# Optimization experiments

Measured on AMD Instinct MI355X. Metric: run time of the kernel, lower is better.

Reference implementation:

```python
import jax, jax.numpy as jnp
import numpy as np

NUM_SAMPLES = 10
MIN_DIST_PTS = 8
TOP_K = 10
GRID_SIZE = 4
GAP = 0.1


def sample_line_points(seg):
    # seg: [N,2,2] (endpoints, ij coords). Vectorized version of the per-group linspace loop.
    lengths = jnp.linalg.norm(seg[:, 0] - seg[:, 1], axis=1)
    n_samp = jnp.clip(jnp.floor(lengths / MIN_DIST_PTS), 2, NUM_SAMPLES)  # [N]
    t = jnp.arange(NUM_SAMPLES, dtype=seg.dtype)  # [S]
    interval = (seg[:, 1] - seg[:, 0]) / (n_samp[:, None] - 1)  # [N,2]
    pts = seg[:, None, 0, :] + t[None, :, None] * interval[:, None, :]  # [N,S,2]
    valid = t[None, :] < n_samp[:, None]  # [N,S]
    pts = jnp.where(valid[..., None], pts, 0.0)  # original zero-pads invalid samples
    return pts, valid


def grid_sample_norm(desc, pts, img_size):
    # desc: [D,Hc,Wc]; pts: [P,2] (i,j) pixel coords in image of size img_size=(H,W).
    # Replicates kornia normalize_pixel_coordinates + F.grid_sample(align_corners=False,
    # bilinear, zero padding), then L2-normalize along D.
    D, Hc, Wc = desc.shape
    H, W = img_size
    gx = 2.0 * pts[:, 1] / (W - 1) - 1.0
    gy = 2.0 * pts[:, 0] / (H - 1) - 1.0
    ix = ((gx + 1.0) * Wc - 1.0) / 2.0
    iy = ((gy + 1.0) * Hc - 1.0) / 2.0
    x0 = jnp.floor(ix)
    y0 = jnp.floor(iy)
    wx1 = ix - x0
    wy1 = iy - y0
    x0i = x0.astype(jnp.int32)
    y0i = y0.astype(jnp.int32)

    def gather(yi, xi):
        inb = (xi >= 0) & (xi < Wc) & (yi >= 0) & (yi < Hc)
        v = desc[:, jnp.clip(yi, 0, Hc - 1), jnp.clip(xi, 0, Wc - 1)]  # [D,P]
        return v * inb

    v = (gather(y0i, x0i) * (1 - wy1) * (1 - wx1)
         + gather(y0i, x0i + 1) * (1 - wy1) * wx1
         + gather(y0i + 1, x0i) * wy1 * (1 - wx1)
         + gather(y0i + 1, x0i + 1) * wy1 * wx1)
    nrm = jnp.linalg.norm(v, axis=0, keepdims=True)
    return v / jnp.maximum(nrm, 1e-12)


def needleman_wunsch(scores):
    # scores: [B,n,m]. Row-wise scan; the within-row dependency
    # v[j+1]=max(v[j], max(prev[j+1], prev[j]+s)) is a prefix-max (cummax).
    b, n, m = scores.shape
    s = scores - GAP
    init = jnp.zeros((b, m + 1), s.dtype)

    def step(prev, row):  # prev [B,m+1], row [B,m]
        a = jnp.maximum(prev[:, 1:], prev[:, :-1] + row)
        new = jnp.maximum(jax.lax.cummax(a, axis=1), 0.0)
        return jnp.concatenate([jnp.zeros((b, 1), s.dtype), new], axis=1), None

    final, _ = jax.lax.scan(step, init, jnp.swapaxes(s, 0, 1))
    return final[:, -1]


def nw_candidate_scores(scores):
    # scores: [N1,N2,S,S] -> (nw [N1,2k], topk [N1,k])
    ls1 = jnp.max(scores, axis=3)
    v1 = ls1 != -1
    ls1 = jnp.where(v1, ls1, 0.0).sum(2) / v1.sum(2)
    ls2 = jnp.max(scores, axis=2)
    v2 = ls2 != -1
    ls2 = jnp.where(v2, ls2, 0.0).sum(2) / v2.sum(2)
    line_scores = (ls1 + ls2) / 2
    topk = jnp.argsort(line_scores, axis=1)[:, -TOP_K:]  # [N1,k]
    top_scores = jnp.take_along_axis(scores, topk[:, :, None, None], axis=1)  # [N1,k,S,S]
    top_scores = jnp.concatenate([top_scores, jnp.flip(top_scores, axis=-1)], axis=1)  # [N1,2k,S,S]
    N1, t2k, n, m = top_scores.shape
    nw = needleman_wunsch(top_scores.reshape(N1 * t2k, n, m)).reshape(N1, t2k)
    return nw, topk


def filter_and_match(scores):
    nw, topk = nw_candidate_scores(scores)
    t2k = nw.shape[1]
    best = jnp.argmax(nw, axis=1) % (t2k // 2)
    return jnp.take_along_axis(topk, best[:, None], axis=1)[:, 0]


def compute_scores(line_seg1, line_seg2, desc1, desc2):
    S = NUM_SAMPLES
    img1 = (desc1.shape[2] * GRID_SIZE, desc1.shape[3] * GRID_SIZE)
    img2 = (desc2.shape[2] * GRID_SIZE, desc2.shape[3] * GRID_SIZE)
    pts1, val1 = sample_line_points(line_seg1)
    pts2, val2 = sample_line_points(line_seg2)
    d1 = grid_sample_norm(desc1[0], pts1.reshape(-1, 2), img1)  # [D, N1*S]
    d2 = grid_sample_norm(desc2[0], pts2.reshape(-1, 2), img2)  # [D, N2*S]
    sc = d1.T @ d2  # [N1*S, N2*S]
    sc = jnp.where(val1.reshape(-1)[:, None], sc, -1.0)
    sc = jnp.where(val2.reshape(-1)[None, :], sc, -1.0)
    N1, N2 = line_seg1.shape[0], line_seg2.shape[0]
    return sc.reshape(N1, S, N2, S).transpose(0, 2, 1, 3)  # [N1,N2,S,S]


def reference(line_seg1, line_seg2, desc1, desc2):
    scores = compute_scores(line_seg1, line_seg2, desc1, desc2)
    matches = filter_and_match(scores)
    # cross check
    matches2 = filter_and_match(scores.transpose(1, 0, 3, 2))
    mutual = matches2[matches] == jnp.arange(line_seg1.shape[0])
    return jnp.where(mutual, matches, -1).astype(jnp.int32)


def setup_inputs() -> dict:
    key = jax.random.key(0)
    k1, k2, k3, k4 = jax.random.split(key, 4)
    IMG = 512.0
    line_seg1 = jax.random.uniform(k1, (512, 2, 2), dtype=jnp.float32) * (IMG - 1.0)
    line_seg2 = jax.random.uniform(k2, (512, 2, 2), dtype=jnp.float32) * (IMG - 1.0)
    desc1 = jax.random.normal(k3, (1, 128, 128, 128), dtype=jnp.float32)
    desc2 = jax.random.normal(k4, (1, 128, 128, 128), dtype=jnp.float32)
    return {"line_seg1": line_seg1, "line_seg2": line_seg2, "desc1": desc1, "desc2": desc2}
```

## Files before the change

kernel.cpp:

```cpp
#include <hip/hip_runtime.h>
#include <cmath>

#define NL 512
#define SS 10
#define DD 128
#define HWC (128 * 128)

typedef _Float16 f16x8 __attribute__((ext_vector_type(8)));
typedef float f32x4 __attribute__((ext_vector_type(4)));

__device__ __forceinline__ void gload_lds16(const void* g, void* l)
{
    __builtin_amdgcn_global_load_lds(
        (__attribute__((address_space(1))) void*)const_cast<void*>(g),
        (__attribute__((address_space(3))) void*)l, 16, 0, 0);
}

__global__ __launch_bounds__(256) void transpose_kernel(
    const float* __restrict__ in1, const float* __restrict__ in2,
    float* __restrict__ out1, float* __restrict__ out2, int* __restrict__ cnt)
{
    if (blockIdx.x == 0 && blockIdx.y == 0 && blockIdx.z == 0 &&
        threadIdx.x == 0 && threadIdx.y == 0)
        atomicExch(cnt, 0);
    const float* in = blockIdx.z ? in2 : in1;
    float* out = blockIdx.z ? out2 : out1;
    __shared__ float tile[32][33];
    int hw0 = blockIdx.x * 32;
    int d0 = blockIdx.y * 32;
    int tx = threadIdx.x, ty = threadIdx.y;
#pragma unroll
    for (int j = 0; j < 32; j += 8)
        tile[ty + j][tx] = in[(size_t)(d0 + ty + j) * HWC + hw0 + tx];
    __syncthreads();
#pragma unroll
    for (int j = 0; j < 32; j += 8)
        out[(size_t)(hw0 + ty + j) * DD + d0 + tx] = tile[tx][ty + j];
}

__device__ __forceinline__ float fetchd(const float* __restrict__ dt, int y, int x, int d)
{
    bool inb = (x >= 0) && (x < 128) && (y >= 0) && (y < 128);
    int yc = y < 0 ? 0 : (y > 127 ? 127 : y);
    int xc = x < 0 ? 0 : (x > 127 ? 127 : x);
    float v = dt[((size_t)(yc * 128 + xc)) * DD + d];
    return inb ? v : 0.0f;
}

__global__ __launch_bounds__(640) void sample_kernel(
    const float* __restrict__ seg1, const float* __restrict__ seg2,
    const float* __restrict__ dt1, const float* __restrict__ dt2,
    float* __restrict__ dd1, float* __restrict__ dd2,
    _Float16* __restrict__ h1, _Float16* __restrict__ m1,
    _Float16* __restrict__ h2, _Float16* __restrict__ m2,
    int* __restrict__ v1, int* __restrict__ v2)
{
#pragma clang fp contract(off)
    int L = blockIdx.x;
    int img = blockIdx.y;
    const float* seg = img ? seg2 : seg1;
    const float* dt = img ? dt2 : dt1;
    float* dd = img ? dd2 : dd1;
    _Float16* ph = img ? h2 : h1;
    _Float16* pm = img ? m2 : m1;
    int* vv = img ? v2 : v1;

    float p0y = seg[L * 4 + 0], p0x = seg[L * 4 + 1];
    float p1y = seg[L * 4 + 2], p1x = seg[L * 4 + 3];
    float dy = p0y - p1y, dx = p0x - p1x;
    float len = sqrtf(dy * dy + dx * dx);
    float nf = floorf(len / 8.0f);
    nf = fminf(fmaxf(nf, 2.0f), 10.0f);
    int ni = (int)nf;
    float ivy = (p1y - p0y) / (nf - 1.0f);
    float ivx = (p1x - p0x) / (nf - 1.0f);

    int t = threadIdx.x >> 6;
    int lane = threadIdx.x & 63;
    int pt = L * SS + t;
    bool val = t < ni;
    int d0 = lane, d1 = lane + 64;
    float o0 = 0.0f, o1 = 0.0f;
    if (val) {
        float py = p0y + (float)t * ivy;
        float px = p0x + (float)t * ivx;
        float gx = 2.0f * px / 511.0f - 1.0f;
        float gy = 2.0f * py / 511.0f - 1.0f;
        float ix = ((gx + 1.0f) * 128.0f - 1.0f) / 2.0f;
        float iy = ((gy + 1.0f) * 128.0f - 1.0f) / 2.0f;
        float x0f = floorf(ix), y0f = floorf(iy);
        float wx = ix - x0f, wy = iy - y0f;
        int x0 = (int)x0f, y0 = (int)y0f;
        float a00 = fetchd(dt, y0, x0, d0),         b00 = fetchd(dt, y0, x0, d1);
        float a01 = fetchd(dt, y0, x0 + 1, d0),     b01 = fetchd(dt, y0, x0 + 1, d1);
        float a10 = fetchd(dt, y0 + 1, x0, d0),     b10 = fetchd(dt, y0 + 1, x0, d1);
        float a11 = fetchd(dt, y0 + 1, x0 + 1, d0), b11 = fetchd(dt, y0 + 1, x0 + 1, d1);
        float omwx = 1.0f - wx, omwy = 1.0f - wy;
        float va = a00 * omwy * omwx + a01 * omwy * wx + a10 * wy * omwx + a11 * wy * wx;
        float vb = b00 * omwy * omwx + b01 * omwy * wx + b10 * wy * omwx + b11 * wy * wx;
        float s = va * va + vb * vb;
#pragma unroll
        for (int m = 1; m < 64; m <<= 1) s += __shfl_xor(s, m);
        float nrm = sqrtf(s);
        o0 = va / fmaxf(nrm, 1e-12f);
        o1 = vb / fmaxf(nrm, 1e-12f);
    }
    dd[(size_t)pt * DD + d0] = o0;
    dd[(size_t)pt * DD + d1] = o1;
    float xs0 = o0 * 256.0f;
    _Float16 hh0 = (_Float16)xs0;
    _Float16 mm0 = (_Float16)(xs0 - (float)hh0);
    float xs1 = o1 * 256.0f;
    _Float16 hh1 = (_Float16)xs1;
    _Float16 mm1 = (_Float16)(xs1 - (float)hh1);
    int po0 = ((pt >> 4) << 11) + ((d0 >> 3) << 7) + ((pt & 15) << 3) + (d0 & 7);
    int po1 = ((pt >> 4) << 11) + ((d1 >> 3) << 7) + ((pt & 15) << 3) + (d1 & 7);
    ph[po0] = hh0; pm[po0] = mm0;
    ph[po1] = hh1; pm[po1] = mm1;
    if (lane == 0) vv[pt] = val ? 1 : 0;
}

__device__ __forceinline__ void stage_ks(
    const _Float16* __restrict__ ah, const _Float16* __restrict__ am,
    const _Float16* __restrict__ bh, const _Float16* __restrict__ bm,
    int bi, int bj, int ks, int wave, int lane, char* dst)
{
#pragma unroll
    for (int c = 0; c < 10; ++c) {
        int chunk = wave * 10 + c;
        int side = chunk >= 20;
        int rem = side ? chunk - 20 : chunk;
        int plane = rem >= 10;
        int pb = plane ? rem - 10 : rem;
        const _Float16* base = side ? (plane ? bm : bh) : (plane ? am : ah);
        size_t off = ((size_t)((side ? bj : bi) * 10 + pb) << 11) + (ks << 9) + (lane << 3);
        gload_lds16(base + off, dst + (chunk << 10));
    }
}

__global__ __launch_bounds__(256, 2) void gemm_ls_kernel(
    const _Float16* __restrict__ ah_, const _Float16* __restrict__ am_,
    const _Float16* __restrict__ bh_, const _Float16* __restrict__ bm_,
    const int* __restrict__ v1, const int* __restrict__ v2,
    float* __restrict__ ls, float* __restrict__ lsT)
{
    __shared__ __align__(16) char smem[122880];
    int tid = threadIdx.x;
    int wave = tid >> 6, lane = tid & 63;
    int wr = wave >> 1, wc = wave & 1;

    int flat = blockIdx.x;
    int xcd = flat & 7, n = flat >> 3;
    int bi = (xcd >> 1) * 8 + (n >> 4);
    int bj = (xcd & 1) * 16 + (n & 15);

    int fro = ((lane >> 4) << 8) + ((lane & 15) << 4);

    f32x4 zz = {0.0f, 0.0f, 0.0f, 0.0f};
    f32x4 acc[5][5];
#pragma unroll
    for (int i = 0; i < 5; ++i)
#pragma unroll
        for (int j = 0; j < 5; ++j) acc[i][j] = zz;

    stage_ks(ah_, am_, bh_, bm_, bi, bj, 0, wave, lane, smem);
    stage_ks(ah_, am_, bh_, bm_, bi, bj, 1, wave, lane, smem + 40960);

#pragma unroll 1
    for (int ks = 0; ks < 4; ++ks) {
        char* buf = smem + 40960 * (ks % 3);
        if (ks < 2) {
            stage_ks(ah_, am_, bh_, bm_, bi, bj, ks + 2, wave, lane,
                     smem + 40960 * ((ks + 2) % 3));
            asm volatile("s_waitcnt vmcnt(20)" ::: "memory");
        } else if (ks == 2) {
            asm volatile("s_waitcnt vmcnt(10)" ::: "memory");
        } else {
            asm volatile("s_waitcnt vmcnt(0)" ::: "memory");
        }
        __builtin_amdgcn_sched_barrier(0);
        __builtin_amdgcn_s_barrier();
        __builtin_amdgcn_sched_barrier(0);

        f16x8 B0[5], B1[5];
#pragma unroll
        for (int j = 0; j < 5; ++j) {
            int pb = wc * 5 + j;
            B0[j] = *(const f16x8*)(buf + ((20 + pb) << 10) + fro);
            B1[j] = *(const f16x8*)(buf + ((30 + pb) << 10) + fro);
        }
#pragma unroll
        for (int i = 0; i < 5; ++i) {
            int pb = wr * 5 + i;
            f16x8 fh = *(const f16x8*)(buf + (pb << 10) + fro);
            f16x8 fm = *(const f16x8*)(buf + ((10 + pb) << 10) + fro);
#pragma unroll
            for (int j = 0; j < 5; ++j) {
                f32x4 t = acc[i][j];
                t = __builtin_amdgcn_mfma_f32_16x16x32_f16(fh, B0[j], t, 0, 0, 0);
                t = __builtin_amdgcn_mfma_f32_16x16x32_f16(fh, B1[j], t, 0, 0, 0);
                t = __builtin_amdgcn_mfma_f32_16x16x32_f16(fm, B0[j], t, 0, 0, 0);
                acc[i][j] = t;
            }
        }
        __builtin_amdgcn_sched_barrier(0);
        __builtin_amdgcn_s_barrier();
        __builtin_amdgcn_sched_barrier(0);
    }

    float* scr = (float*)smem;
    const float rescale = 1.0f / 65536.0f;
    for (int half = 0; half < 2; ++half) {
        __syncthreads();
        if (wr == half) {
            float* reg = scr + wc * 6464;
#pragma unroll
            for (int i = 0; i < 5; ++i)
#pragma unroll
                for (int j = 0; j < 5; ++j)
#pragma unroll
                    for (int r = 0; r < 4; ++r) {
                        int row = i * 16 + ((lane >> 4) << 2) + r;
                        int col = j * 16 + (lane & 15);
                        int pi = row / 10, s = row - pi * 10;
                        int pj = col / 10, t = col - pj * 10;
                        reg[(pi * 8 + pj) * 101 + s * 10 + t] = acc[i][j][r] * rescale;
                    }
            asm volatile("s_waitcnt lgkmcnt(0)" ::: "memory");
            const float* mp = reg + lane * 101;
            int iL = bi * 16 + half * 8 + (lane >> 3);
            int jL = bj * 16 + wc * 8 + (lane & 7);
            int va[10], vb[10];
#pragma unroll
            for (int s = 0; s < 10; ++s) va[s] = v1[iL * 10 + s];
#pragma unroll
            for (int t = 0; t < 10; ++t) vb[t] = v2[jL * 10 + t];
            float cmx[10];
#pragma unroll
            for (int t = 0; t < 10; ++t) cmx[t] = -3.0e38f;
            float sum1 = 0.0f; int c1 = 0;
#pragma unroll
            for (int s = 0; s < 10; ++s) {
                float rmx = -3.0e38f;
#pragma unroll
                for (int t = 0; t < 10; ++t) {
                    float v = (va[s] && vb[t]) ? mp[s * 10 + t] : -1.0f;
                    rmx = fmaxf(rmx, v);
                    cmx[t] = fmaxf(cmx[t], v);
                }
                if (rmx != -1.0f) { sum1 += rmx; c1++; }
            }
            float sum2 = 0.0f; int c2 = 0;
#pragma unroll
            for (int t = 0; t < 10; ++t) {
                if (cmx[t] != -1.0f) { sum2 += cmx[t]; c2++; }
            }
            float out = (sum1 / (float)c1 + sum2 / (float)c2) * 0.5f;
            ls[(size_t)iL * NL + jL] = out;
            lsT[(size_t)jL * NL + iL] = out;
        }
    }
}

__global__ __launch_bounds__(256) void nw_kernel(
    const float* __restrict__ d1, const float* __restrict__ d2,
    const int* __restrict__ v1, const int* __restrict__ v2,
    const float* __restrict__ ls, const float* __restrict__ lsT,
    int* __restrict__ topkg, float* __restrict__ nwout,
    int* __restrict__ cnt, int* __restrict__ outg)
{
    int L = blockIdx.x;
    int dir = blockIdx.y;
    const float* Ad = dir ? d2 : d1;
    const float* Bd = dir ? d1 : d2;
    const int* vA = dir ? v2 : v1;
    const int* vB = dir ? v1 : v2;
    const float* src = dir ? &lsT[(size_t)L * NL] : &ls[(size_t)L * NL];

    __shared__ float Asl[10 * 132];
    __shared__ float Bsl[10][1320];
    __shared__ float M[10][110];
    __shared__ int vam[10], tks[10];
    __shared__ int lastflag;
    __shared__ int m1f[NL], m2f[NL];

    int tid = threadIdx.x;
    if (tid < 10) vam[tid] = vA[L * 10 + tid];
#pragma unroll
    for (int it = 0; it < 5; ++it) {
        int idx = tid + it * 256;
        int row = idx >> 7, col = idx & 127;
        Asl[row * 132 + col] = Ad[((size_t)L * 10 + row) * DD + col];
    }
    if (tid < 64) {
        int lane = tid;
        float v[8];
#pragma unroll
        for (int it = 0; it < 8; ++it) v[it] = src[it * 64 + lane];
        for (int p = 9; p >= 0; --p) {
            float bv = -3.0e38f;
            int bi_ = -1;
#pragma unroll
            for (int it = 0; it < 8; ++it) {
                int j = it * 64 + lane;
                bool better = (v[it] > bv) || (v[it] == bv && j > bi_);
                if (better) { bv = v[it]; bi_ = j; }
            }
#pragma unroll
            for (int m = 1; m < 64; m <<= 1) {
                float ov = __shfl_xor(bv, m);
                int oi = __shfl_xor(bi_, m);
                bool better = (ov > bv) || (ov == bv && oi > bi_);
                if (better) { bv = ov; bi_ = oi; }
            }
            if ((bi_ & 63) == lane) v[bi_ >> 6] = -3.0e38f;
            if (lane == 0) tks[p] = bi_;
        }
    }
    __syncthreads();
    if (tid < 10) topkg[(size_t)(dir * NL + L) * 10 + tid] = tks[tid];
#pragma unroll
    for (int it = 0; it < 50; ++it) {
        int idx = tid + it * 256;
        int c = idx / 1280;
        int rem = idx - c * 1280;
        int row = rem >> 7, col = rem & 127;
        Bsl[c][row * 132 + col] = Bd[((size_t)tks[c] * 10 + row) * DD + col];
    }
    __syncthreads();
#pragma unroll
    for (int it = 0; it < 4; ++it) {
        int w = tid + it * 256;
        if (w < 1000) {
            int c = w / 100;
            int rem = w - c * 100;
            int s = rem / 10, t = rem - s * 10;
            const float4* ap = (const float4*)&Asl[s * 132];
            const float4* bp = (const float4*)&Bsl[c][t * 132];
            float acc = 0.0f;
#pragma unroll
            for (int k = 0; k < 32; ++k) {
                float4 a = ap[k], b = bp[k];
                acc = fmaf(a.x, b.x, acc);
                acc = fmaf(a.y, b.y, acc);
                acc = fmaf(a.z, b.z, acc);
                acc = fmaf(a.w, b.w, acc);
            }
            int ok = vam[s] && vB[tks[c] * 10 + t];
            M[c][s * 11 + t] = ok ? acc : -1.0f;
        }
    }
    __syncthreads();

    if (tid < 20) {
        int c = tid % 10, f = tid / 10;
        float prev[11];
#pragma unroll
        for (int p = 0; p < 11; ++p) prev[p] = 0.0f;
#pragma unroll
        for (int s = 0; s < 10; ++s) {
            float oldp = prev[0];
            float run = -3.0e38f;
#pragma unroll
            for (int t = 0; t < 10; ++t) {
                int tt = f ? (9 - t) : t;
                float sc = M[c][s * 11 + tt] - 0.1f;
                float pt1 = prev[t + 1];
                float av = fmaxf(pt1, oldp + sc);
                run = fmaxf(run, av);
                prev[t + 1] = fmaxf(run, 0.0f);
                oldp = pt1;
            }
        }
        nwout[((size_t)(dir * NL + L)) * 20 + f * 10 + c] = prev[10];
    }
    __syncthreads();
    if (tid == 0) {
        __threadfence();
        lastflag = (atomicAdd(cnt, 1) == 2 * NL - 1) ? 1 : 0;
    }
    __syncthreads();
    if (!lastflag) return;

    __threadfence();
#pragma unroll
    for (int rep = 0; rep < 2; ++rep) {
        int t = tid + rep * 256;
        {
            const float* p = nwout + (size_t)t * 20;
            float bb = -3.0e38f; int kk = 0;
            for (int k = 0; k < 20; ++k) {
                float v = p[k];
                if (v > bb) { bb = v; kk = k; }
            }
            m1f[t] = topkg[(size_t)t * 10 + (kk % 10)];
        }
        {
            const float* p = nwout + (size_t)(NL + t) * 20;
            float bb = -3.0e38f; int kk = 0;
            for (int k = 0; k < 20; ++k) {
                float v = p[k];
                if (v > bb) { bb = v; kk = k; }
            }
            m2f[t] = topkg[(size_t)(NL + t) * 10 + (kk % 10)];
        }
    }
    __syncthreads();
#pragma unroll
    for (int rep = 0; rep < 2; ++rep) {
        int t = tid + rep * 256;
        int mt = m1f[t];
        outg[t] = (m2f[mt] == t) ? mt : -1;
    }
}

extern "C" void kernel_launch(void* const* d_in, const int* in_sizes, int n_in,
                              void* d_out, int out_size, void* d_ws, size_t ws_size,
                              hipStream_t stream)
{
    const float* seg1 = (const float*)d_in[0];
    const float* seg2 = (const float*)d_in[1];
    const float* desc1 = (const float*)d_in[2];
    const float* desc2 = (const float*)d_in[3];
    int* out = (int*)d_out;

    char* ws = (char*)d_ws;
    size_t off = 0;
    float* dt1 = (float*)(ws + off); off += (size_t)DD * HWC * 4;
    float* dt2 = (float*)(ws + off); off += (size_t)DD * HWC * 4;
    float* dd1 = (float*)(ws + off); off += (size_t)NL * SS * DD * 4;
    float* dd2 = (float*)(ws + off); off += (size_t)NL * SS * DD * 4;
    int* v1 = (int*)(ws + off); off += (size_t)NL * SS * 4;
    int* v2 = (int*)(ws + off); off += (size_t)NL * SS * 4;
    float* ls = (float*)(ws + off); off += (size_t)NL * NL * 4;
    float* lsT = (float*)(ws + off); off += (size_t)NL * NL * 4;
    int* topk = (int*)(ws + off); off += (size_t)2 * NL * 10 * 4;
    float* nwv = (float*)(ws + off); off += (size_t)2 * NL * 20 * 4;
    int* cnt = (int*)(ws + off); off += 256;
    size_t PL = (size_t)NL * SS * DD;
    _Float16* h1 = (_Float16*)(ws + off); off += PL * 2;
    _Float16* m1 = (_Float16*)(ws + off); off += PL * 2;
    _Float16* h2 = (_Float16*)(ws + off); off += PL * 2;
    _Float16* m2 = (_Float16*)(ws + off); off += PL * 2;

    transpose_kernel<<<dim3(HWC / 32, DD / 32, 2), dim3(32, 8), 0, stream>>>(
        desc1, desc2, dt1, dt2, cnt);
    sample_kernel<<<dim3(NL, 2), 640, 0, stream>>>(
        seg1, seg2, dt1, dt2, dd1, dd2, h1, m1, h2, m2, v1, v2);
    gemm_ls_kernel<<<1024, 256, 0, stream>>>(
        h1, m1, h2, m2, v1, v2, ls, lsT);
    nw_kernel<<<dim3(NL, 2), 256, 0, stream>>>(
        dd1, dd2, v1, v2, ls, lsT, topk, nwv, cnt, out);
}
```

Baseline: 174.5 us.

## Prefetch all GEMM k-stages up front and split NW candidates across two blocks

The GEMM kernel enlarges shared memory so all four k-slices are loaded at kernel start, removing buffer rotation and one barrier per iteration; this raises LDS use and likely cuts occupancy to one block per CU. The NW kernel adds a grid z-dimension that splits the ten top-k candidates into two blocks of five, doubling parallelism but repeating the top-k selection in each block. The dot-product loop uses four independent accumulators to shorten the FMA dependency chain, and the completion counter threshold is updated for the larger grid.

Result: slower. 199.7 us (+14.5%).

```diff
diff --git a/kernel.cpp b/kernel.cpp
--- a/kernel.cpp
+++ b/kernel.cpp
@@ -144,7 +144,7 @@
     const int* __restrict__ v1, const int* __restrict__ v2,
     float* __restrict__ ls, float* __restrict__ lsT)
 {
-    __shared__ __align__(16) char smem[122880];
+    __shared__ __align__(16) char smem[163840];
     int tid = threadIdx.x;
     int wave = tid >> 6, lane = tid & 63;
     int wr = wave >> 1, wc = wave & 1;
@@ -163,20 +163,18 @@
 #pragma unroll
         for (int j = 0; j < 5; ++j) acc[i][j] = zz;
 
-    stage_ks(ah_, am_, bh_, bm_, bi, bj, 0, wave, lane, smem);
-    stage_ks(ah_, am_, bh_, bm_, bi, bj, 1, wave, lane, smem + 40960);
+#pragma unroll
+    for (int ks = 0; ks < 4; ++ks)
+        stage_ks(ah_, am_, bh_, bm_, bi, bj, ks, wave, lane, smem + 40960 * ks);
 
 #pragma unroll 1
     for (int ks = 0; ks < 4; ++ks) {
-        char* buf = smem + 40960 * (ks % 3);
-        if (ks < 2) {
-            stage_ks(ah_, am_, bh_, bm_, bi, bj, ks + 2, wave, lane,
-                     smem + 40960 * ((ks + 2) % 3));
-            asm volatile("s_waitcnt vmcnt(20)" ::: "memory");
-        } else if (ks == 2) {
-            asm volatile("s_waitcnt vmcnt(10)" ::: "memory");
-        } else {
-            asm volatile("s_waitcnt vmcnt(0)" ::: "memory");
+        char* buf = smem + 40960 * ks;
+        switch (ks) {
+            case 0: asm volatile("s_waitcnt vmcnt(30)" ::: "memory"); break;
+            case 1: asm volatile("s_waitcnt vmcnt(20)" ::: "memory"); break;
+            case 2: asm volatile("s_waitcnt vmcnt(10)" ::: "memory"); break;
+            default: asm volatile("s_waitcnt vmcnt(0)" ::: "memory"); break;
         }
         __builtin_amdgcn_sched_barrier(0);
         __builtin_amdgcn_s_barrier();
@@ -203,9 +201,6 @@
                 acc[i][j] = t;
             }
         }
-        __builtin_amdgcn_sched_barrier(0);
-        __builtin_amdgcn_s_barrier();
-        __builtin_amdgcn_sched_barrier(0);
     }
 
     float* scr = (float*)smem;
@@ -271,6 +266,7 @@
 {
     int L = blockIdx.x;
     int dir = blockIdx.y;
+    int cg = blockIdx.z;
     const float* Ad = dir ? d2 : d1;
     const float* Bd = dir ? d1 : d2;
     const int* vA = dir ? v2 : v1;
@@ -278,8 +274,8 @@
     const float* src = dir ? &lsT[(size_t)L * NL] : &ls[(size_t)L * NL];
 
     __shared__ float Asl[10 * 132];
-    __shared__ float Bsl[10][1320];
-    __shared__ float M[10][110];
+    __shared__ float Bsl[5][1320];
+    __shared__ float M[5][110];
     __shared__ int vam[10], tks[10];
     __shared__ int lastflag;
     __shared__ int m1f[NL], m2f[NL];
@@ -318,42 +314,50 @@
         }
     }
     __syncthreads();
-    if (tid < 10) topkg[(size_t)(dir * NL + L) * 10 + tid] = tks[tid];
-#pragma unroll
-    for (int it = 0; it < 50; ++it) {
+    if (cg == 0 && tid < 10) topkg[(size_t)(dir * NL + L) * 10 + tid] = tks[tid];
+#pragma unroll
+    for (int it = 0; it < 25; ++it) {
         int idx = tid + it * 256;
         int c = idx / 1280;
         int rem = idx - c * 1280;
         int row = rem >> 7, col = rem & 127;
-        Bsl[c][row * 132 + col] = Bd[((size_t)tks[c] * 10 + row) * DD + col];
-    }
-    __syncthreads();
-#pragma unroll
-    for (int it = 0; it < 4; ++it) {
+        Bsl[c][row * 132 + col] = Bd[((size_t)tks[cg * 5 + c] * 10 + row) * DD + col];
+    }
+    __syncthreads();
+#pragma unroll
+    for (int it = 0; it < 2; ++it) {
         int w = tid + it * 256;
-        if (w < 1000) {
+        if (w < 500) {
             int c = w / 100;
             int rem = w - c * 100;
             int s = rem / 10, t = rem - s * 10;
             const float4* ap = (const float4*)&Asl[s * 132];
             const float4* bp = (const float4*)&Bsl[c][t * 132];
-            float acc = 0.0f;
-#pragma unroll
-            for (int k = 0; k < 32; ++k) {
-                float4 a = ap[k], b = bp[k];
-                acc = fmaf(a.x, b.x, acc);
-                acc = fmaf(a.y, b.y, acc);
-                acc = fmaf(a.z, b.z, acc);
-                acc = fmaf(a.w, b.w, acc);
-            }
-            int ok = vam[s] && vB[tks[c] * 10 + t];
-            M[c][s * 11 + t] = ok ? acc : -1.0f;
-        }
-    }
-    __syncthreads();
-
-    if (tid < 20) {
-        int c = tid % 10, f = tid / 10;
+            float a0 = 0.0f, a1 = 0.0f, a2 = 0.0f, a3 = 0.0f;
+#pragma unroll
+            for (int k = 0; k < 32; k += 4) {
+                float4 x0 = ap[k], y0 = bp[k];
+                a0 = fmaf(x0.x, y0.x, a0); a0 = fmaf(x0.y, y0.y, a0);
+                a0 = fmaf(x0.z, y0.z, a0); a0 = fmaf(x0.w, y0.w, a0);
+                float4 x1 = ap[k + 1], y1 = bp[k + 1];
+                a1 = fmaf(x1.x, y1.x, a1); a1 = fmaf(x1.y, y1.y, a1);
+                a1 = fmaf(x1.z, y1.z, a1); a1 = fmaf(x1.w, y1.w, a1);
+                float4 x2 = ap[k + 2], y2 = bp[k + 2];
+                a2 = fmaf(x2.x, y2.x, a2); a2 = fmaf(x2.y, y2.y, a2);
+                a2 = fmaf(x2.z, y2.z, a2); a2 = fmaf(x2.w, y2.w, a2);
+                float4 x3 = ap[k + 3], y3 = bp[k + 3];
+                a3 = fmaf(x3.x, y3.x, a3); a3 = fmaf(x3.y, y3.y, a3);
+                a3 = fmaf(x3.z, y3.z, a3); a3 = fmaf(x3.w, y3.w, a3);
+            }
+            float accv = (a0 + a1) + (a2 + a3);
+            int ok = vam[s] && vB[tks[cg * 5 + c] * 10 + t];
+            M[c][s * 11 + t] = ok ? accv : -1.0f;
+        }
+    }
+    __syncthreads();
+
+    if (tid < 10) {
+        int c = tid % 5, f = tid / 5;
         float prev[11];
 #pragma unroll
         for (int p = 0; p < 11; ++p) prev[p] = 0.0f;
@@ -372,12 +376,12 @@
                 oldp = pt1;
             }
         }
-        nwout[((size_t)(dir * NL + L)) * 20 + f * 10 + c] = prev[10];
+        nwout[((size_t)(dir * NL + L)) * 20 + f * 10 + cg * 5 + c] = prev[10];
     }
     __syncthreads();
     if (tid == 0) {
         __threadfence();
-        lastflag = (atomicAdd(cnt, 1) == 2 * NL - 1) ? 1 : 0;
+        lastflag = (atomicAdd(cnt, 1) == 4 * NL - 1) ? 1 : 0;
     }
     __syncthreads();
     if (!lastflag) return;
@@ -449,6 +453,6 @@
         seg1, seg2, dt1, dt2, dd1, dd2, h1, m1, h2, m2, v1, v2);
     gemm_ls_kernel<<<1024, 256, 0, stream>>>(
         h1, m1, h2, m2, v1, v2, ls, lsT);
-    nw_kernel<<<dim3(NL, 2), 256, 0, stream>>>(
+    nw_kernel<<<dim3(NL, 2, 2), 256, 0, stream>>>(
         dd1, dd2, v1, v2, ls, lsT, topk, nwv, cnt, out);
 }
```
